# Performance work log

Measured on AMD Instinct MI355X. Metric: run time of the kernel, lower is better.

The kernel has to match this reference:

```python
import jax, jax.numpy as jnp
import numpy as np

VOCAB = 50265
D = 768
NUM_ROLES = 12
CODE_DEFAULT = 255 - 1  # fallback valid length for code
NL_DEFAULT = 127 - 1    # fallback valid length for nl


def _l2norm(x, eps=1e-12):
    n = jnp.sqrt(jnp.sum(x * x, axis=-1, keepdims=True))
    return x / jnp.maximum(n, eps)


def _valid_mask(ids, default_len):
    # first position where token == 2 (eos); if none, use default_len
    is2 = ids == 2
    has2 = jnp.any(is2, axis=1)
    first = jnp.argmax(is2, axis=1)
    total = jnp.where(has2, first, default_len)  # [B]
    S = ids.shape[1]
    return (jnp.arange(S)[None, :] < total[:, None]).astype(jnp.float32)


def setup_inputs() -> dict:
    key = jax.random.key(0)
    ks = jax.random.split(key, 12)
    B, Sc, Sn = 64, 640, 128
    code_inputs = jax.random.randint(ks[0], (B, Sc), 0, VOCAB)
    attn_mask = jax.random.randint(ks[1], (B, Sc, Sc), 0, 2).astype(bool)
    position_idx = jax.random.randint(ks[2], (B, Sc), 0, 5)
    nl_inputs = jax.random.randint(ks[3], (B, Sn), 0, VOCAB)
    role_indices = jax.random.randint(ks[4], (B, Sc), 0, NUM_ROLES)
    W_emb = jax.random.normal(ks[5], (VOCAB, D), dtype=jnp.float32) * 0.02
    role_table = jax.random.normal(ks[6], (NUM_ROLES, D), dtype=jnp.float32) * 0.02
    w_code = jax.random.normal(ks[7], (D,), dtype=jnp.float32) * 0.02
    b_code = jnp.zeros((), dtype=jnp.float32)
    w_nl = jax.random.normal(ks[8], (D,), dtype=jnp.float32) * 0.02
    b_nl = jnp.zeros((), dtype=jnp.float32)
    return {
        "code_inputs": code_inputs, "attn_mask": attn_mask,
        "position_idx": position_idx, "nl_inputs": nl_inputs,
        "role_indices": role_indices, "W_emb": W_emb,
        "role_table": role_table, "w_code": w_code, "b_code": b_code,
        "w_nl": w_nl, "b_nl": b_nl,
    }


def reference(code_inputs, attn_mask, position_idx, nl_inputs, role_indices,
              W_emb, role_table, w_code, b_code, w_nl, b_nl):
    # ---- code branch: DFG-node aggregation over code tokens ----
    nodes_mask = position_idx == 0            # [B,Sc] DFG nodes
    token_mask = position_idx >= 2            # [B,Sc] code tokens
    emb = W_emb[code_inputs]                  # [B,Sc,D]
    # dense node->token mask (the memory-bound tensor)
    m = (nodes_mask[:, :, None] & token_mask[:, None, :] & attn_mask).astype(emb.dtype)
    m = m / (jnp.sum(m, axis=-1, keepdims=True) + 1e-10)
    avg = jnp.einsum('bnt,btd->bnd', m, emb)  # masked-mean token embeddings per node
    mixed = jnp.where(nodes_mask[:, :, None], avg, emb)
    # encoder treated as identity (black-box HF encoder); custom math is faithful
    code_hidden = _l2norm(mixed)
    code_hwr = code_hidden + role_table[role_indices]
    code_probs = jax.nn.sigmoid(jnp.einsum('bsd,d->bs', code_hwr, w_code) + b_code)
    code_probs = code_probs * _valid_mask(code_inputs, CODE_DEFAULT)
    # ---- nl branch ----
    nl_hidden = _l2norm(W_emb[nl_inputs])
    nl_probs = jax.nn.sigmoid(jnp.einsum('bsd,d->bs', nl_hidden, w_nl) + b_nl)
    nl_probs = nl_probs * _valid_mask(nl_inputs, NL_DEFAULT)
    # ---- similarity matrix ----
    sim_mat = jnp.einsum('bnd,bmd->bnm', nl_hidden, code_hidden)  # [B,Sn,Sc]
    return (code_hidden, code_probs, nl_hidden, nl_probs, sim_mat)
```

## Files before the change

kernel.cpp:

```cpp
#include <hip/hip_runtime.h>

#define BB 64
#define SC 640
#define SN 128
#define DD 768
#define CODE_DEF 254
#define NL_DEF 126

typedef short bf16x8 __attribute__((ext_vector_type(8)));
typedef float f32x4 __attribute__((ext_vector_type(4)));

__device__ __forceinline__ unsigned short f2bf(float f) {
  unsigned u = __float_as_uint(f);
  u += 0x7fffu + ((u >> 16) & 1u);
  return (unsigned short)(u >> 16);
}

__global__ __launch_bounds__(64) void k0_prep(
    const int* __restrict__ code_ids, const int* __restrict__ nl_ids,
    const int* __restrict__ pos, const unsigned* __restrict__ attn_u32,
    int* __restrict__ nn, int* __restrict__ node_idx,
    int* __restrict__ len_code, int* __restrict__ len_nl,
    int* __restrict__ flag) {
  int b = blockIdx.x;
  int lane = threadIdx.x;
  int first = CODE_DEF;
  for (int c = 0; c < SC; c += 64) {
    bool is2 = code_ids[b * SC + c + lane] == 2;
    unsigned long long m = __ballot(is2);
    if (m) { first = c + __builtin_ctzll(m); break; }
  }
  int firstn = NL_DEF;
  for (int c = 0; c < SN; c += 64) {
    bool is2 = nl_ids[b * SN + c + lane] == 2;
    unsigned long long m = __ballot(is2);
    if (m) { firstn = c + __builtin_ctzll(m); break; }
  }
  int base = 0;
  for (int c = 0; c < SC; c += 64) {
    bool isn = pos[b * SC + c + lane] == 0;
    unsigned long long m = __ballot(isn);
    int pre = __popcll(m & ((1ull << lane) - 1ull));
    if (isn) node_idx[b * SC + base + pre] = c + lane;
    base += __popcll(m);
  }
  if (lane == 0) { nn[b] = base; len_code[b] = first; len_nl[b] = firstn; }
  if (b == 0) {
    int bad = 0;
    for (int i = lane; i < 1024; i += 64)
      if (attn_u32[i] > 1u) bad = 1;
    unsigned long long m = __ballot(bad);
    if (lane == 0) flag[0] = (m != 0ull) ? 1 : 0;
  }
}

__global__ __launch_bounds__(256) void k0b_mask(
    const int* __restrict__ attn, const int* __restrict__ pos,
    const int* __restrict__ nn, const int* __restrict__ node_idx,
    const int* __restrict__ flag,
    unsigned long long* __restrict__ mbits64, float* __restrict__ counts) {
  int id = blockIdx.x;
  int b = id & 63, g = id >> 6;
  int w = threadIdx.x >> 6, lane = threadIdx.x & 63;
  int count = nn[b];
  int isu8 = flag[0];
  for (int rr = 0; rr < 4; ++rr) {
    int slot = g * 16 + w * 4 + rr;
    long obase = ((long)b * 256 + slot) * 10;
    if (slot >= count) {
      if (lane < 10) mbits64[obase + lane] = 0ull;
      if (lane == 0) counts[b * 256 + slot] = 0.f;
      continue;
    }
    int nrow = node_idx[b * SC + slot];
    int tot = 0;
    for (int k = 0; k < 10; ++k) {
      int t = k * 64 + lane;
      bool tk = pos[b * SC + t] >= 2;
      bool av;
      if (isu8)
        av = ((const unsigned char*)attn)[((long)b * SC + nrow) * SC + t] != 0;
      else
        av = attn[((long)b * SC + nrow) * SC + t] != 0;
      unsigned long long m = __ballot(av && tk);
      if (lane == 0) mbits64[obase + k] = m;
      tot += __popcll(m);
    }
    if (lane == 0) counts[b * 256 + slot] = (float)tot;
  }
}

__global__ __launch_bounds__(256) void k2_mfma(
    const unsigned* __restrict__ mbits, const float* __restrict__ counts,
    const int* __restrict__ nn, const int* __restrict__ node_idx,
    const int* __restrict__ code_ids, const float* __restrict__ Wemb,
    float* __restrict__ codeh) {
  __shared__ unsigned short As[2][128 * 64];
  __shared__ unsigned short Bs[2][128 * 64];
  __shared__ int rowsidx[128];
  __shared__ int cid[SC];
  int id = blockIdx.x;
  int b = id & 63;
  int g = id >> 6;
  int ntile = g / 6, dtile = g % 6;
  int count = nn[b];
  if (ntile * 128 >= count) return;
  int tid = threadIdx.x;
  for (int i = tid; i < SC; i += 256) cid[i] = code_ids[b * SC + i];
  if (tid < 128) {
    int slot = ntile * 128 + tid;
    rowsidx[tid] = (slot < count) ? node_idx[b * SC + slot] : -1;
  }
  __syncthreads();
  const int lane = tid & 63, w = tid >> 6, wm = w >> 1, wn = w & 1;
  const int dcol = dtile * 128;

  f32x4 acc[4][4];
#pragma unroll
  for (int m = 0; m < 4; ++m)
#pragma unroll
    for (int n = 0; n < 4; ++n) acc[m][n] = (f32x4){0.f, 0.f, 0.f, 0.f};

  const int r_ = tid >> 1, h_ = tid & 1;
  const unsigned* mrow = mbits + ((long)b * 256 + ntile * 128 + r_) * 20;
  int tg4[2], d0[2];
#pragma unroll
  for (int q = 0; q < 2; ++q) {
    int task = tid + 256 * q;
    tg4[q] = task >> 5;
    d0[q] = (task & 31) * 4;
  }

  f32x4 va[2][4];
  unsigned bitsv;

#define LOADC(cc)                                                         \
  {                                                                       \
    bitsv = mrow[(cc) * 2 + h_];                                          \
    _Pragma("unroll") for (int q = 0; q < 2; ++q)                         \
        _Pragma("unroll") for (int j = 0; j < 4; ++j) va[q][j] =          \
        *(const f32x4*)(Wemb +                                            \
                        (long)cid[(cc) * 64 + tg4[q] * 4 + j] * DD +      \
                        dcol + d0[q]);                                    \
  }

#define WRITEB(bf_)                                                       \
  {                                                                       \
    unsigned short* Ab = As[bf_];                                         \
    unsigned short* Bb = Bs[bf_];                                         \
    _Pragma("unroll") for (int gg = 0; gg < 4; ++gg) {                    \
      int tl = h_ * 32 + gg * 8;                                          \
      bf16x8 u;                                                           \
      _Pragma("unroll") for (int j = 0; j < 8; ++j) u[j] =                \
          ((bitsv >> (gg * 8 + j)) & 1u) ? (short)0x3F80 : (short)0;      \
      *(bf16x8*)(&Ab[r_ * 64 + (tl ^ ((r_ & 7) << 3))]) = u;              \
    }                                                                     \
    _Pragma("unroll") for (int q = 0; q < 2; ++q)                         \
        _Pragma("unroll") for (int dj = 0; dj < 4; ++dj) {                \
      int d = d0[q] + dj;                                                 \
      ushort4 u = {f2bf(va[q][0][dj]), f2bf(va[q][1][dj]),                \
                   f2bf(va[q][2][dj]), f2bf(va[q][3][dj])};               \
      int s = ((((d >> 2) & 7) ^ ((d & 3) << 1)) << 3);                   \
      *(ushort4*)(&Bb[d * 64 + ((tg4[q] * 4) ^ s)]) = u;                  \
    }                                                                     \
  }

#define MFMAP(bf_)                                                        \
  {                                                                       \
    const unsigned short* Ab = As[bf_];                                   \
    const unsigned short* Bb = Bs[bf_];                                   \
    _Pragma("unroll") for (int ks = 0; ks < 2; ++ks) {                    \
      int kb = ks * 32 + (lane >> 4) * 8;                                 \
      bf16x8 af[4], bfv[4];                                               \
      _Pragma("unroll") for (int m = 0; m < 4; ++m) {                     \
        int rr = wm * 64 + m * 16 + (lane & 15);                          \
        af[m] = *(const bf16x8*)(&Ab[rr * 64 + (kb ^ ((rr & 7) << 3))]);  \
      }                                                                   \
      _Pragma("unroll") for (int n = 0; n < 4; ++n) {                     \
        int cc = wn * 64 + n * 16 + (lane & 15);                          \
        int s = ((((cc >> 2) & 7) ^ ((cc & 3) << 1)) << 3);               \
        bfv[n] = *(const bf16x8*)(&Bb[cc * 64 + (kb ^ s)]);               \
      }                                                                   \
      _Pragma("unroll") for (int m = 0; m < 4; ++m)                       \
          _Pragma("unroll") for (int n = 0; n < 4; ++n) acc[m][n] =       \
          __builtin_amdgcn_mfma_f32_16x16x32_bf16(af[m], bfv[n],          \
                                                  acc[m][n], 0, 0, 0);    \
    }                                                                     \
  }

  LOADC(0);
  WRITEB(0);
  __syncthreads();
  for (int c = 0; c < 10; ++c) {
    if (c < 9) LOADC(c + 1);
    MFMAP(c & 1);
    if (c < 9) WRITEB((c + 1) & 1);
    __syncthreads();
  }

  float* outb = codeh + (long)b * SC * DD + dcol + wn * 64;
#pragma unroll
  for (int m = 0; m < 4; ++m) {
    int row0 = wm * 64 + m * 16 + ((lane >> 4) << 2);
#pragma unroll
    for (int rr2 = 0; rr2 < 4; ++rr2) {
      int slotr = row0 + rr2;
      int nr = rowsidx[slotr];
      if (nr < 0) continue;
      float cnt = counts[b * 256 + ntile * 128 + slotr];
      float inv = (cnt > 0.f) ? 1.f / cnt : 0.f;
      float* orow = outb + (long)nr * DD;
#pragma unroll
      for (int n = 0; n < 4; ++n)
        orow[n * 16 + (lane & 15)] = acc[m][n][rr2] * inv;
    }
  }
#undef LOADC
#undef WRITEB
#undef MFMAP
}

__global__ __launch_bounds__(256) void k3_fused(
    const int* __restrict__ code_ids, const int* __restrict__ pos,
    const float* __restrict__ Wemb, float* __restrict__ codeh,
    const int* __restrict__ roles, const float* __restrict__ role_table,
    const float* __restrict__ w_code, const float* __restrict__ b_code,
    const int* __restrict__ len_code, float* __restrict__ code_probs) {
  int w = threadIdx.x >> 6, lane = threadIdx.x & 63;
  long row = (long)blockIdx.x * 4 + w;
  int b = (int)(row / SC), s = (int)(row % SC);
  float* rp = codeh + row * DD;
  const float* src =
      (pos[row] == 0) ? rp : (Wemb + (long)code_ids[row] * DD);
  f32x4 x[3];
#pragma unroll
  for (int j = 0; j < 3; ++j)
    x[j] = *(const f32x4*)(src + lane * 4 + j * 256);
  float ss = 0.f;
#pragma unroll
  for (int j = 0; j < 3; ++j)
#pragma unroll
    for (int e = 0; e < 4; ++e) ss += x[j][e] * x[j][e];
#pragma unroll
  for (int o = 32; o > 0; o >>= 1) ss += __shfl_xor(ss, o, 64);
  float inv = 1.f / fmaxf(sqrtf(ss), 1e-12f);
  const float* rt = role_table + (long)roles[row] * DD;
  float dot = 0.f;
#pragma unroll
  for (int j = 0; j < 3; ++j) {
    f32x4 r = *(const f32x4*)(rt + lane * 4 + j * 256);
    f32x4 wc = *(const f32x4*)(w_code + lane * 4 + j * 256);
    f32x4 y;
#pragma unroll
    for (int e = 0; e < 4; ++e) {
      y[e] = x[j][e] * inv;
      dot += (y[e] + r[e]) * wc[e];
    }
    *(f32x4*)(rp + lane * 4 + j * 256) = y;
  }
#pragma unroll
  for (int o = 32; o > 0; o >>= 1) dot += __shfl_xor(dot, o, 64);
  if (lane == 0) {
    float p = 1.f / (1.f + expf(-(dot + b_code[0])));
    code_probs[row] = (s < len_code[b]) ? p : 0.f;
  }
}

__global__ __launch_bounds__(256) void k4_nl(
    const int* __restrict__ ids, const float* __restrict__ Wemb,
    const float* __restrict__ w_nl, const float* __restrict__ b_nl,
    const int* __restrict__ len_nl, float* __restrict__ nlh,
    float* __restrict__ nl_probs) {
  int w = threadIdx.x >> 6, lane = threadIdx.x & 63;
  long row = (long)blockIdx.x * 4 + w;
  int b = (int)(row / SN), s = (int)(row % SN);
  const float* src = Wemb + (long)ids[row] * DD;
  f32x4 x[3];
#pragma unroll
  for (int j = 0; j < 3; ++j)
    x[j] = *(const f32x4*)(src + lane * 4 + j * 256);
  float ss = 0.f;
#pragma unroll
  for (int j = 0; j < 3; ++j)
#pragma unroll
    for (int e = 0; e < 4; ++e) ss += x[j][e] * x[j][e];
#pragma unroll
  for (int o = 32; o > 0; o >>= 1) ss += __shfl_xor(ss, o, 64);
  float inv = 1.f / fmaxf(sqrtf(ss), 1e-12f);
  float* o = nlh + row * DD;
  float dot = 0.f;
#pragma unroll
  for (int j = 0; j < 3; ++j) {
    f32x4 wn = *(const f32x4*)(w_nl + lane * 4 + j * 256);
    f32x4 y;
#pragma unroll
    for (int e = 0; e < 4; ++e) {
      y[e] = x[j][e] * inv;
      dot += y[e] * wn[e];
    }
    *(f32x4*)(o + lane * 4 + j * 256) = y;
  }
#pragma unroll
  for (int of = 32; of > 0; of >>= 1) dot += __shfl_xor(dot, of, 64);
  if (lane == 0) {
    float p = 1.f / (1.f + expf(-(dot + b_nl[0])));
    nl_probs[row] = (s < len_nl[b]) ? p : 0.f;
  }
}

__global__ __launch_bounds__(256) void k5_mfma(const float* __restrict__ nlh,
                                               const float* __restrict__ codeh,
                                               float* __restrict__ sim) {
  __shared__ unsigned short As[128 * 64];
  __shared__ unsigned short Bs[128 * 64];
  int id = blockIdx.x;
  int b = id & 63;
  int ct = id >> 6;
  int tid = threadIdx.x;
  int lane = tid & 63;
  int w = tid >> 6;
  int wm = w >> 1, wn = w & 1;

  f32x4 acc[4][4];
#pragma unroll
  for (int m = 0; m < 4; ++m)
#pragma unroll
    for (int n = 0; n < 4; ++n) acc[m][n] = (f32x4){0.f, 0.f, 0.f, 0.f};

  const float* Ag = nlh + (long)b * SN * DD;
  const float* Bg = codeh + ((long)b * SC + ct * 128) * DD;

  for (int c = 0; c < DD / 64; ++c) {
#pragma unroll
    for (int it = 0; it < 8; ++it) {
      int i = tid + 256 * it;
      int row = i >> 4;
      int k0 = (i & 15) * 4;
      int sk = k0 ^ ((row & 7) << 3);
      float4 vaa = *(const float4*)(Ag + (long)row * DD + c * 64 + k0);
      ushort4 ua;
      ua.x = f2bf(vaa.x); ua.y = f2bf(vaa.y); ua.z = f2bf(vaa.z); ua.w = f2bf(vaa.w);
      *(ushort4*)(&As[row * 64 + sk]) = ua;
      float4 vbb = *(const float4*)(Bg + (long)row * DD + c * 64 + k0);
      ushort4 ub;
      ub.x = f2bf(vbb.x); ub.y = f2bf(vbb.y); ub.z = f2bf(vbb.z); ub.w = f2bf(vbb.w);
      *(ushort4*)(&Bs[row * 64 + sk]) = ub;
    }
    __syncthreads();
#pragma unroll
    for (int ks = 0; ks < 2; ++ks) {
      int kb = ks * 32 + (lane >> 4) * 8;
      bf16x8 af[4], bfr[4];
#pragma unroll
      for (int m = 0; m < 4; ++m) {
        int rr = wm * 64 + m * 16 + (lane & 15);
        af[m] = *(const bf16x8*)(&As[rr * 64 + (kb ^ ((rr & 7) << 3))]);
      }
#pragma unroll
      for (int n = 0; n < 4; ++n) {
        int rr = wn * 64 + n * 16 + (lane & 15);
        bfr[n] = *(const bf16x8*)(&Bs[rr * 64 + (kb ^ ((rr & 7) << 3))]);
      }
#pragma unroll
      for (int m = 0; m < 4; ++m)
#pragma unroll
        for (int n = 0; n < 4; ++n)
          acc[m][n] = __builtin_amdgcn_mfma_f32_16x16x32_bf16(
              af[m], bfr[n], acc[m][n], 0, 0, 0);
    }
    __syncthreads();
  }
  long ob = (long)b * SN * SC + (long)ct * 128;
#pragma unroll
  for (int m = 0; m < 4; ++m) {
    int row0 = wm * 64 + m * 16 + ((lane >> 4) << 2);
#pragma unroll
    for (int n = 0; n < 4; ++n) {
      int col = wn * 64 + n * 16 + (lane & 15);
#pragma unroll
      for (int rr = 0; rr < 4; ++rr)
        sim[ob + (long)(row0 + rr) * SC + col] = acc[m][n][rr];
    }
  }
}

extern "C" void kernel_launch(void* const* d_in, const int* in_sizes, int n_in,
                              void* d_out, int out_size, void* d_ws,
                              size_t ws_size, hipStream_t stream) {
  const int* code_ids = (const int*)d_in[0];
  const int* attn = (const int*)d_in[1];
  const int* pos = (const int*)d_in[2];
  const int* nl_ids = (const int*)d_in[3];
  const int* roles = (const int*)d_in[4];
  const float* Wemb = (const float*)d_in[5];
  const float* role_table = (const float*)d_in[6];
  const float* w_code = (const float*)d_in[7];
  const float* b_code = (const float*)d_in[8];
  const float* w_nl = (const float*)d_in[9];
  const float* b_nl = (const float*)d_in[10];

  float* out = (float*)d_out;
  float* codeh = out;
  float* code_probs = out + 31457280;
  float* nlh = out + 31498240;
  float* nl_probs = out + 37789696;
  float* sim = out + 37797888;

  int* wsi = (int*)d_ws;
  int* nn = wsi;
  int* node_idx = wsi + 64;
  int* len_code = node_idx + BB * SC;
  int* len_nl = len_code + 64;
  int* flag = len_nl + 64;
  unsigned* mbits = (unsigned*)(wsi + 49152);
  float* counts = (float*)(wsi + 49152 + 327680);

  k0_prep<<<BB, 64, 0, stream>>>(code_ids, nl_ids, pos, (const unsigned*)attn,
                                 nn, node_idx, len_code, len_nl, flag);
  k0b_mask<<<BB * 16, 256, 0, stream>>>(attn, pos, nn, node_idx, flag,
                                        (unsigned long long*)mbits, counts);
  k4_nl<<<BB * SN / 4, 256, 0, stream>>>(nl_ids, Wemb, w_nl, b_nl, len_nl, nlh,
                                         nl_probs);
  k2_mfma<<<BB * 12, 256, 0, stream>>>(mbits, counts, nn, node_idx, code_ids,
                                       Wemb, codeh);
  k3_fused<<<BB * SC / 4, 256, 0, stream>>>(code_ids, pos, Wemb, codeh, roles,
                                            role_table, w_code, b_code,
                                            len_code, code_probs);
  k5_mfma<<<BB * (SC / 128), 256, 0, stream>>>(nlh, codeh, sim);
}
```

Before: 174.8 us.

## Pre-transpose gathered embeddings to bf16 blob and split sim GEMM tiles

Adds a kernel that gathers code-token embeddings, converts them to bf16, and writes a pre-transposed blob laid out per (batch, 64-token chunk). The aggregation GEMM then streams B tiles straight from that blob instead of gathering fp32 rows and converting inside the loop. This removes the in-loop gather and conversion but drops double buffering and adds an extra global write and read pass. Separately, the similarity GEMM splits the 128 NL rows into two 64-row tiles, doubling the grid to raise occupancy, at the cost of loading code tiles twice.

Measured after the change: 220.3 us. 1.26x slower.

```diff
diff --git a/kernel.cpp b/kernel.cpp
--- a/kernel.cpp
+++ b/kernel.cpp
@@ -90,15 +90,47 @@
   }
 }
 
+#define TPAD 132
+__global__ __launch_bounds__(256) void kT_blob(
+    const int* __restrict__ code_ids, const float* __restrict__ Wemb,
+    unsigned short* __restrict__ blob) {
+  __shared__ float T[64][TPAD];
+  __shared__ int cid_l[64];
+  int id = blockIdx.x;
+  int b = id & 63, c = id >> 6;
+  int tid = threadIdx.x;
+  if (tid < 64) cid_l[tid] = code_ids[b * SC + c * 64 + tid];
+  __syncthreads();
+  unsigned short* ob = blob + (long)(b * 10 + c) * (DD * 64);
+  for (int p = 0; p < 6; ++p) {
+    int col4 = (tid & 31) * 4;
+#pragma unroll
+    for (int it = 0; it < 8; ++it) {
+      int row = it * 8 + (tid >> 5);
+      f32x4 v = *(const f32x4*)(Wemb + (long)cid_l[row] * DD + p * 128 + col4);
+      *(f32x4*)(&T[row][col4]) = v;
+    }
+    __syncthreads();
+#pragma unroll
+    for (int it2 = 0; it2 < 4; ++it2) {
+      int task = tid + 256 * it2;
+      int dl = task >> 3, tg = task & 7;
+      bf16x8 u;
+#pragma unroll
+      for (int j = 0; j < 8; ++j) u[j] = (short)f2bf(T[tg * 8 + j][dl]);
+      *(bf16x8*)(ob + (long)(p * 128 + dl) * 64 + tg * 8) = u;
+    }
+    __syncthreads();
+  }
+}
+
 __global__ __launch_bounds__(256) void k2_mfma(
     const unsigned* __restrict__ mbits, const float* __restrict__ counts,
     const int* __restrict__ nn, const int* __restrict__ node_idx,
-    const int* __restrict__ code_ids, const float* __restrict__ Wemb,
-    float* __restrict__ codeh) {
-  __shared__ unsigned short As[2][128 * 64];
-  __shared__ unsigned short Bs[2][128 * 64];
+    const unsigned short* __restrict__ blob, float* __restrict__ codeh) {
+  __shared__ unsigned short As[128 * 64];
+  __shared__ unsigned short Bs[128 * 64];
   __shared__ int rowsidx[128];
-  __shared__ int cid[SC];
   int id = blockIdx.x;
   int b = id & 63;
   int g = id >> 6;
@@ -106,14 +138,11 @@
   int count = nn[b];
   if (ntile * 128 >= count) return;
   int tid = threadIdx.x;
-  for (int i = tid; i < SC; i += 256) cid[i] = code_ids[b * SC + i];
   if (tid < 128) {
     int slot = ntile * 128 + tid;
     rowsidx[tid] = (slot < count) ? node_idx[b * SC + slot] : -1;
   }
-  __syncthreads();
   const int lane = tid & 63, w = tid >> 6, wm = w >> 1, wn = w & 1;
-  const int dcol = dtile * 128;
 
   f32x4 acc[4][4];
 #pragma unroll
@@ -123,82 +152,53 @@
 
   const int r_ = tid >> 1, h_ = tid & 1;
   const unsigned* mrow = mbits + ((long)b * 256 + ntile * 128 + r_) * 20;
-  int tg4[2], d0[2];
-#pragma unroll
-  for (int q = 0; q < 2; ++q) {
-    int task = tid + 256 * q;
-    tg4[q] = task >> 5;
-    d0[q] = (task & 31) * 4;
-  }
-
-  f32x4 va[2][4];
-  unsigned bitsv;
-
-#define LOADC(cc)                                                         \
-  {                                                                       \
-    bitsv = mrow[(cc) * 2 + h_];                                          \
-    _Pragma("unroll") for (int q = 0; q < 2; ++q)                         \
-        _Pragma("unroll") for (int j = 0; j < 4; ++j) va[q][j] =          \
-        *(const f32x4*)(Wemb +                                            \
-                        (long)cid[(cc) * 64 + tg4[q] * 4 + j] * DD +      \
-                        dcol + d0[q]);                                    \
-  }
-
-#define WRITEB(bf_)                                                       \
-  {                                                                       \
-    unsigned short* Ab = As[bf_];                                         \
-    unsigned short* Bb = Bs[bf_];                                         \
-    _Pragma("unroll") for (int gg = 0; gg < 4; ++gg) {                    \
-      int tl = h_ * 32 + gg * 8;                                          \
-      bf16x8 u;                                                           \
-      _Pragma("unroll") for (int j = 0; j < 8; ++j) u[j] =                \
-          ((bitsv >> (gg * 8 + j)) & 1u) ? (short)0x3F80 : (short)0;      \
-      *(bf16x8*)(&Ab[r_ * 64 + (tl ^ ((r_ & 7) << 3))]) = u;              \
-    }                                                                     \
-    _Pragma("unroll") for (int q = 0; q < 2; ++q)                         \
-        _Pragma("unroll") for (int dj = 0; dj < 4; ++dj) {                \
-      int d = d0[q] + dj;                                                 \
-      ushort4 u = {f2bf(va[q][0][dj]), f2bf(va[q][1][dj]),                \
-                   f2bf(va[q][2][dj]), f2bf(va[q][3][dj])};               \
-      int s = ((((d >> 2) & 7) ^ ((d & 3) << 1)) << 3);                   \
-      *(ushort4*)(&Bb[d * 64 + ((tg4[q] * 4) ^ s)]) = u;                  \
-    }                                                                     \
-  }
-
-#define MFMAP(bf_)                                                        \
-  {                                                                       \
-    const unsigned short* Ab = As[bf_];                                   \
-    const unsigned short* Bb = Bs[bf_];                                   \
-    _Pragma("unroll") for (int ks = 0; ks < 2; ++ks) {                    \
-      int kb = ks * 32 + (lane >> 4) * 8;                                 \
-      bf16x8 af[4], bfv[4];                                               \
-      _Pragma("unroll") for (int m = 0; m < 4; ++m) {                     \
-        int rr = wm * 64 + m * 16 + (lane & 15);                          \
-        af[m] = *(const bf16x8*)(&Ab[rr * 64 + (kb ^ ((rr & 7) << 3))]);  \
-      }                                                                   \
-      _Pragma("unroll") for (int n = 0; n < 4; ++n) {                     \
-        int cc = wn * 64 + n * 16 + (lane & 15);                          \
-        int s = ((((cc >> 2) & 7) ^ ((cc & 3) << 1)) << 3);               \
-        bfv[n] = *(const bf16x8*)(&Bb[cc * 64 + (kb ^ s)]);               \
-      }                                                                   \
-      _Pragma("unroll") for (int m = 0; m < 4; ++m)                       \
-          _Pragma("unroll") for (int n = 0; n < 4; ++n) acc[m][n] =       \
-          __builtin_amdgcn_mfma_f32_16x16x32_bf16(af[m], bfv[n],          \
-                                                  acc[m][n], 0, 0, 0);    \
-    }                                                                     \
-  }
-
-  LOADC(0);
-  WRITEB(0);
-  __syncthreads();
+
   for (int c = 0; c < 10; ++c) {
-    if (c < 9) LOADC(c + 1);
-    MFMAP(c & 1);
-    if (c < 9) WRITEB((c + 1) & 1);
-    __syncthreads();
-  }
-
-  float* outb = codeh + (long)b * SC * DD + dcol + wn * 64;
+    const unsigned short* src =
+        blob + (long)(b * 10 + c) * (DD * 64) + dtile * (128 * 64);
+    unsigned bitsv = mrow[c * 2 + h_];
+#pragma unroll
+    for (int it = 0; it < 4; ++it) {
+      int task = tid + 256 * it;
+      int drow = task >> 3, tg = task & 7;
+      bf16x8 v = *(const bf16x8*)(src + drow * 64 + tg * 8);
+      *(bf16x8*)(&Bs[drow * 64 + ((tg * 8) ^ ((drow & 7) << 3))]) = v;
+    }
+#pragma unroll
+    for (int gg = 0; gg < 4; ++gg) {
+      int tl = h_ * 32 + gg * 8;
+      bf16x8 u;
+#pragma unroll
+      for (int j = 0; j < 8; ++j)
+        u[j] = ((bitsv >> (gg * 8 + j)) & 1u) ? (short)0x3F80 : (short)0;
+      *(bf16x8*)(&As[r_ * 64 + (tl ^ ((r_ & 7) << 3))]) = u;
+    }
+    __syncthreads();
+#pragma unroll
+    for (int ks = 0; ks < 2; ++ks) {
+      int kb = ks * 32 + (lane >> 4) * 8;
+      bf16x8 af[4], bfv[4];
+#pragma unroll
+      for (int m = 0; m < 4; ++m) {
+        int rr = wm * 64 + m * 16 + (lane & 15);
+        af[m] = *(const bf16x8*)(&As[rr * 64 + (kb ^ ((rr & 7) << 3))]);
+      }
+#pragma unroll
+      for (int n = 0; n < 4; ++n) {
+        int cc = wn * 64 + n * 16 + (lane & 15);
+        bfv[n] = *(const bf16x8*)(&Bs[cc * 64 + (kb ^ ((cc & 7) << 3))]);
+      }
+#pragma unroll
+      for (int m = 0; m < 4; ++m)
+#pragma unroll
+        for (int n = 0; n < 4; ++n)
+          acc[m][n] = __builtin_amdgcn_mfma_f32_16x16x32_bf16(af[m], bfv[n],
+                                                              acc[m][n], 0, 0, 0);
+    }
+    __syncthreads();
+  }
+
+  float* outb = codeh + (long)b * SC * DD + dtile * 128 + wn * 64;
 #pragma unroll
   for (int m = 0; m < 4; ++m) {
     int row0 = wm * 64 + m * 16 + ((lane >> 4) << 2);
@@ -215,9 +215,6 @@
         orow[n * 16 + (lane & 15)] = acc[m][n][rr2] * inv;
     }
   }
-#undef LOADC
-#undef WRITEB
-#undef MFMAP
 }
 
 __global__ __launch_bounds__(256) void k3_fused(
@@ -311,49 +308,51 @@
 __global__ __launch_bounds__(256) void k5_mfma(const float* __restrict__ nlh,
                                                const float* __restrict__ codeh,
                                                float* __restrict__ sim) {
-  __shared__ unsigned short As[128 * 64];
+  __shared__ unsigned short As[64 * 64];
   __shared__ unsigned short Bs[128 * 64];
   int id = blockIdx.x;
   int b = id & 63;
-  int ct = id >> 6;
+  int r = id >> 6;
+  int nt = r % 2, ct = r / 2;
   int tid = threadIdx.x;
   int lane = tid & 63;
   int w = tid >> 6;
   int wm = w >> 1, wn = w & 1;
 
-  f32x4 acc[4][4];
-#pragma unroll
-  for (int m = 0; m < 4; ++m)
+  f32x4 acc[2][4];
+#pragma unroll
+  for (int m = 0; m < 2; ++m)
 #pragma unroll
     for (int n = 0; n < 4; ++n) acc[m][n] = (f32x4){0.f, 0.f, 0.f, 0.f};
 
-  const float* Ag = nlh + (long)b * SN * DD;
+  const float* Ag = nlh + ((long)b * SN + nt * 64) * DD;
   const float* Bg = codeh + ((long)b * SC + ct * 128) * DD;
 
   for (int c = 0; c < DD / 64; ++c) {
+#pragma unroll
+    for (int it = 0; it < 4; ++it) {
+      int i = tid + 256 * it;
+      int row = i >> 4, k0 = (i & 15) * 4;
+      float4 va = *(const float4*)(Ag + (long)row * DD + c * 64 + k0);
+      ushort4 ua = {f2bf(va.x), f2bf(va.y), f2bf(va.z), f2bf(va.w)};
+      *(ushort4*)(&As[row * 64 + (k0 ^ ((row & 7) << 3))]) = ua;
+    }
 #pragma unroll
     for (int it = 0; it < 8; ++it) {
       int i = tid + 256 * it;
-      int row = i >> 4;
-      int k0 = (i & 15) * 4;
-      int sk = k0 ^ ((row & 7) << 3);
-      float4 vaa = *(const float4*)(Ag + (long)row * DD + c * 64 + k0);
-      ushort4 ua;
-      ua.x = f2bf(vaa.x); ua.y = f2bf(vaa.y); ua.z = f2bf(vaa.z); ua.w = f2bf(vaa.w);
-      *(ushort4*)(&As[row * 64 + sk]) = ua;
-      float4 vbb = *(const float4*)(Bg + (long)row * DD + c * 64 + k0);
-      ushort4 ub;
-      ub.x = f2bf(vbb.x); ub.y = f2bf(vbb.y); ub.z = f2bf(vbb.z); ub.w = f2bf(vbb.w);
-      *(ushort4*)(&Bs[row * 64 + sk]) = ub;
+      int row = i >> 4, k0 = (i & 15) * 4;
+      float4 vb = *(const float4*)(Bg + (long)row * DD + c * 64 + k0);
+      ushort4 ub = {f2bf(vb.x), f2bf(vb.y), f2bf(vb.z), f2bf(vb.w)};
+      *(ushort4*)(&Bs[row * 64 + (k0 ^ ((row & 7) << 3))]) = ub;
     }
     __syncthreads();
 #pragma unroll
     for (int ks = 0; ks < 2; ++ks) {
       int kb = ks * 32 + (lane >> 4) * 8;
-      bf16x8 af[4], bfr[4];
-#pragma unroll
-      for (int m = 0; m < 4; ++m) {
-        int rr = wm * 64 + m * 16 + (lane & 15);
+      bf16x8 af[2], bfr[4];
+#pragma unroll
+      for (int m = 0; m < 2; ++m) {
+        int rr = wm * 32 + m * 16 + (lane & 15);
         af[m] = *(const bf16x8*)(&As[rr * 64 + (kb ^ ((rr & 7) << 3))]);
       }
 #pragma unroll
@@ -362,7 +361,7 @@
         bfr[n] = *(const bf16x8*)(&Bs[rr * 64 + (kb ^ ((rr & 7) << 3))]);
       }
 #pragma unroll
-      for (int m = 0; m < 4; ++m)
+      for (int m = 0; m < 2; ++m)
 #pragma unroll
         for (int n = 0; n < 4; ++n)
           acc[m][n] = __builtin_amdgcn_mfma_f32_16x16x32_bf16(
@@ -370,10 +369,10 @@
     }
     __syncthreads();
   }
-  long ob = (long)b * SN * SC + (long)ct * 128;
-#pragma unroll
-  for (int m = 0; m < 4; ++m) {
-    int row0 = wm * 64 + m * 16 + ((lane >> 4) << 2);
+  long ob = ((long)b * SN + nt * 64) * SC + ct * 128;
+#pragma unroll
+  for (int m = 0; m < 2; ++m) {
+    int row0 = wm * 32 + m * 16 + ((lane >> 4) << 2);
 #pragma unroll
     for (int n = 0; n < 4; ++n) {
       int col = wn * 64 + n * 16 + (lane & 15);
@@ -414,17 +413,20 @@
   int* flag = len_nl + 64;
   unsigned* mbits = (unsigned*)(wsi + 49152);
   float* counts = (float*)(wsi + 49152 + 327680);
+  unsigned short* blob =
+      (unsigned short*)((char*)d_ws + (8u << 20));
 
   k0_prep<<<BB, 64, 0, stream>>>(code_ids, nl_ids, pos, (const unsigned*)attn,
                                  nn, node_idx, len_code, len_nl, flag);
   k0b_mask<<<BB * 16, 256, 0, stream>>>(attn, pos, nn, node_idx, flag,
                                         (unsigned long long*)mbits, counts);
+  kT_blob<<<BB * 10, 256, 0, stream>>>(code_ids, Wemb, blob);
   k4_nl<<<BB * SN / 4, 256, 0, stream>>>(nl_ids, Wemb, w_nl, b_nl, len_nl, nlh,
                                          nl_probs);
-  k2_mfma<<<BB * 12, 256, 0, stream>>>(mbits, counts, nn, node_idx, code_ids,
-                                       Wemb, codeh);
+  k2_mfma<<<BB * 12, 256, 0, stream>>>(mbits, counts, nn, node_idx, blob,
+                                       codeh);
   k3_fused<<<BB * SC / 4, 256, 0, stream>>>(code_ids, pos, Wemb, codeh, roles,
                                             role_table, w_code, b_code,
                                             len_code, code_probs);
-  k5_mfma<<<BB * (SC / 128), 256, 0, stream>>>(nlh, codeh, sim);
-}
+  k5_mfma<<<BB * 10, 256, 0, stream>>>(nlh, codeh, sim);
+}
```
